# Kernel tuning notes

Hardware: AMD Instinct MI355X
Metric: run time of the kernel (lower is better)

The kernel has to match this reference:

```python
import jax, jax.numpy as jnp
import numpy as np

H = 4      # num_heads
C = 64     # attention_num_c
C_Z = 128  # num_in_c (pair rep channels)
C_T = 64   # num_in_c_kv (template pair channels)


def setup_inputs() -> dict:
    key = jax.random.key(0)
    ks = jax.random.split(key, 7)
    B, T, R = 1, 4, 384
    z2d = jax.random.normal(ks[0], (B, R, R, C_Z), dtype=jnp.float32)
    t2d = jax.random.normal(ks[1], (B, T, R, R, C_T), dtype=jnp.float32)
    s = 0.02
    Wq = jax.random.normal(ks[2], (C_Z, H * C), dtype=jnp.float32) * s
    Wk = jax.random.normal(ks[3], (C_T, H * C), dtype=jnp.float32) * s
    Wv = jax.random.normal(ks[4], (C_T, H * C), dtype=jnp.float32) * s
    Wo = jax.random.normal(ks[5], (H * C, C_Z), dtype=jnp.float32) * s
    bo = jax.random.normal(ks[6], (C_Z,), dtype=jnp.float32) * s
    return {"z2d": z2d, "t2d": t2d, "Wq": Wq, "Wk": Wk, "Wv": Wv, "Wo": Wo, "bo": bo}


def reference(z2d, t2d, Wq, Wk, Wv, Wo, bo):
    B, R = z2d.shape[0], z2d.shape[-2]
    T = t2d.shape[1]
    P = R * R  # residue-pair axis
    # query: one query per residue pair
    zq = z2d.reshape(B, P, 1, C_Z)
    # templates become the key/value axis per residue pair
    tkv = jnp.transpose(t2d, (0, 2, 3, 1, 4)).reshape(B, P, T, C_T)
    q = (zq @ Wq).reshape(B, P, 1, H, C) * (C ** -0.5)
    k = (tkv @ Wk).reshape(B, P, T, H, C)
    v = (tkv @ Wv).reshape(B, P, T, H, C)
    logits = jnp.einsum('bpqhc,bpkhc->bphqk', q, k)  # [B,P,H,1,T]
    weights = jax.nn.softmax(logits, axis=-1)
    weighted_avg = jnp.einsum('bphqk,bpkhc->bpqhc', weights, v)  # [B,P,1,H,C]
    out = weighted_avg.reshape(B, P, 1, H * C) @ Wo + bo
    return out.reshape(B, R, R, C_Z)
```

## Files before the change

kernel.cpp:

```cpp
#include <hip/hip_runtime.h>


#define R_    384
#define P_    (R_ * R_)
#define PB    32
#define NPB   256
#define NT_   18

typedef __attribute__((ext_vector_type(8))) short  short8;
typedef __attribute__((ext_vector_type(4))) float  f32x4;

union S8U { short8 s8; unsigned u[4]; };

__device__ __forceinline__ unsigned short f2bf(float f) {
  unsigned u = __float_as_uint(f);
  unsigned r = ((u >> 16) & 1u) + 0x7FFFu;
  return (unsigned short)((u + r) >> 16);
}
__device__ __forceinline__ float bf2f(unsigned short s) {
  return __uint_as_float(((unsigned)s) << 16);
}
__device__ __forceinline__ unsigned cvtpk(float lo, float hi) {
  unsigned d;
  asm("v_cvt_pk_bf16_f32 %0, %1, %2" : "=v"(d) : "v"(lo), "v"(hi));
  return d;
}
__device__ __forceinline__ int swz(int p, int c) {
  return p * 256 + ((((c >> 3) ^ (p & 31)) << 3) | (c & 7));
}
#define SB() __builtin_amdgcn_sched_barrier(0)
#define BAR() do { \
    asm volatile("s_waitcnt lgkmcnt(0)\ns_barrier" ::: "memory"); \
    SB(); \
  } while (0)

__device__ __forceinline__ void dma16(const float* g, void* lds) {
  __builtin_amdgcn_global_load_lds((const __attribute__((address_space(1))) unsigned*)g,
                                   (__attribute__((address_space(3))) unsigned*)lds,
                                   16, 0, 0);
}

__global__ void prep_kernel(const float* __restrict__ Wq, const float* __restrict__ Wk,
                            const float* __restrict__ Wv, const float* __restrict__ Wo,
                            unsigned short* __restrict__ AbarT,
                            unsigned short* __restrict__ MbarT) {
  int tid = blockIdx.x * blockDim.x + threadIdx.x;
  if (tid < 256 * 128) {
    int n = tid >> 7, i = tid & 127;
    int h = n >> 6, j = n & 63;
    const float* wq = Wq + i * 256 + h * 64;
    const float* wk = Wk + j * 256 + h * 64;
    float acc = 0.f;
#pragma unroll 8
    for (int c = 0; c < 64; ++c) acc += wq[c] * wk[c];
    AbarT[n * 128 + i] = f2bf(acc * 0.125f);
  } else {
    int t2 = tid - 256 * 128;
    int o = t2 >> 8, k = t2 & 255;
    int h = k >> 6, j = k & 63;
    const float* wv = Wv + j * 256 + h * 64;
    const float* wo = Wo + (h * 64) * 128 + o;
    float acc = 0.f;
#pragma unroll 8
    for (int c = 0; c < 64; ++c) acc += wv[c] * wo[c * 128];
    MbarT[o * 256 + k] = f2bf(acc);
  }
}

__global__ __launch_bounds__(512, 2) void attn_kernel(
    const float* __restrict__ z2d, const float* __restrict__ t2d,
    const unsigned short* __restrict__ AbarT, const unsigned short* __restrict__ MbarT,
    const float* __restrict__ bo, float* __restrict__ out) {
  extern __shared__ char smem[];
  unsigned short* sAbar = (unsigned short*)smem;
  float*          sTf   = (float*)(smem + 65536);
  unsigned short* sG    = (unsigned short*)(smem + 131072);

  const int tid  = threadIdx.x;
  const int wv_  = tid >> 6;
  const int lane = tid & 63;
  const int l = lane & 15;
  const int q = lane >> 4;
  const int mt = wv_ & 1;
  const int ng = wv_ >> 1;

  const int dp  = wv_ * 4 + (lane >> 4);
  const int dcf = (((lane & 15) ^ ((lane >> 4) & 3)) << 2);

  const int ap = tid >> 4, asub = tid & 15;
  const int ah = asub >> 2, au = asub & 3;
  const int aoG0 = swz(ap, ah * 64 + au * 16);
  const int aoG1 = swz(ap, ah * 64 + au * 16 + 8);
  int aoK[4];
#pragma unroll
  for (int j = 0; j < 4; ++j)
    aoK[j] = ap * 64 + ((((au * 4 + j) ^ (ap & 3))) << 2);

  const int p2g = mt * 16 + l;

#pragma unroll
  for (int k2 = 0; k2 < 8; ++k2) {
    int id = k2 * 512 + tid, n = id >> 4, blk = id & 15;
    short8 v = *(const short8*)(AbarT + n * 128 + blk * 8);
    *(short8*)(sAbar + n * 128 + ((blk ^ (n & 15)) << 3)) = v;
  }
  short8 mb0[8], mb1[8];
#pragma unroll
  for (int kk = 0; kk < 8; ++kk) {
    mb0[kk] = *(const short8*)(MbarT + (size_t)(ng * 32 + l) * 256 + kk * 32 + q * 8);
    mb1[kk] = *(const short8*)(MbarT + (size_t)(ng * 32 + 16 + l) * 256 + kk * 32 + q * 8);
  }
  const float bo0 = bo[ng * 32 + l];
  const float bo1 = bo[ng * 32 + 16 + l];
  SB();
  {
    const size_t P00 = (size_t)blockIdx.x * PB;
    char* dst = (char*)sTf + wv_ * 1024;
#pragma unroll
    for (int m = 0; m < 4; ++m)
      dma16(t2d + ((size_t)m * P_ + P00 + dp) * 64 + dcf, dst + m * 8192);
  }
  SB();
  float4 zb[8];
  {
    const float* zr = z2d + ((size_t)blockIdx.x * PB + mt * 16 + l) * 128;
#pragma unroll
    for (int kk = 0; kk < 4; ++kk) {
      zb[2 * kk]     = *(const float4*)(zr + kk * 32 + q * 8);
      zb[2 * kk + 1] = *(const float4*)(zr + kk * 32 + q * 8 + 4);
    }
  }
  BAR();

#pragma unroll 1
  for (int k = 0; k < NT_; ++k) {
    const int sl = k & 1;
    const size_t P0 = (size_t)(blockIdx.x + (size_t)k * NPB) * PB;
    const size_t P0n = P0 + (size_t)NPB * PB;

    if (k + 1 < NT_) {
      char* dst = (char*)sTf + (sl ^ 1) * 32768 + wv_ * 1024;
#pragma unroll
      for (int m = 0; m < 4; ++m)
        dma16(t2d + ((size_t)m * P_ + P0n + dp) * 64 + dcf, dst + m * 8192);
    }
    SB();
    if (k > 0) {
      const unsigned short* sGp = sG + (sl ^ 1) * 8192;
      f32x4 a20 = f32x4{0.f, 0.f, 0.f, 0.f};
      f32x4 a21 = f32x4{0.f, 0.f, 0.f, 0.f};
#pragma unroll
      for (int kk = 0; kk < 8; ++kk) {
        short8 af2 = *(const short8*)(sGp + p2g * 256 + (((kk * 4 + q) ^ p2g) << 3));
        a20 = __builtin_amdgcn_mfma_f32_16x16x32_bf16(af2, mb0[kk], a20, 0, 0, 0);
        a21 = __builtin_amdgcn_mfma_f32_16x16x32_bf16(af2, mb1[kk], a21, 0, 0, 0);
      }
      const size_t rb = (P0 - (size_t)NPB * PB + (size_t)(mt * 16 + q * 4)) * 128;
#pragma unroll
      for (int r = 0; r < 4; ++r) {
        out[rb + r * 128 + ng * 32 + l]      = a20[r] + bo0;
        out[rb + r * 128 + ng * 32 + 16 + l] = a21[r] + bo1;
      }
    }
    SB();
    {
      f32x4 a1[4];
#pragma unroll
      for (int i = 0; i < 4; ++i) a1[i] = f32x4{0.f, 0.f, 0.f, 0.f};
#pragma unroll
      for (int kk = 0; kk < 4; ++kk) {
        S8U af;
        af.u[0] = cvtpk(zb[2 * kk].x,     zb[2 * kk].y);
        af.u[1] = cvtpk(zb[2 * kk].z,     zb[2 * kk].w);
        af.u[2] = cvtpk(zb[2 * kk + 1].x, zb[2 * kk + 1].y);
        af.u[3] = cvtpk(zb[2 * kk + 1].z, zb[2 * kk + 1].w);
#pragma unroll
        for (int i = 0; i < 4; ++i) {
          const int n = (ng * 4 + i) * 16 + l;
          short8 bf = *(const short8*)(sAbar + n * 128 + (((kk * 4 + q) ^ l) << 3));
          a1[i] = __builtin_amdgcn_mfma_f32_16x16x32_bf16(af.s8, bf, a1[i], 0, 0, 0);
        }
      }
      unsigned short* sGc = sG + sl * 8192;
#pragma unroll
      for (int i = 0; i < 4; ++i) {
        const int c = (ng * 4 + i) * 16 + l;
#pragma unroll
        for (int r = 0; r < 4; ++r)
          sGc[swz(mt * 16 + q * 4 + r, c)] = f2bf(a1[i][r]);
      }
    }
    SB();
    if (k + 1 < NT_) {
      const float* zr = z2d + (P0n + (size_t)(mt * 16 + l)) * 128;
#pragma unroll
      for (int kk = 0; kk < 4; ++kk) {
        zb[2 * kk]     = *(const float4*)(zr + kk * 32 + q * 8);
        zb[2 * kk + 1] = *(const float4*)(zr + kk * 32 + q * 8 + 4);
      }
    }
    SB();
    BAR();

    {
      const float* Kt = sTf + sl * 8192;
      unsigned short* sGc = sG + sl * 8192;
      short8 g0 = *(const short8*)(sGc + aoG0);
      short8 g1 = *(const short8*)(sGc + aoG1);
      float lg0 = 0.f, lg1 = 0.f, lg2 = 0.f, lg3 = 0.f;
#pragma unroll
      for (int j = 0; j < 4; ++j) {
        const float ga = bf2f((unsigned short)((j < 2) ? g0[4 * j]     : g1[4 * (j - 2)]));
        const float gb = bf2f((unsigned short)((j < 2) ? g0[4 * j + 1] : g1[4 * (j - 2) + 1]));
        const float gc = bf2f((unsigned short)((j < 2) ? g0[4 * j + 2] : g1[4 * (j - 2) + 2]));
        const float gd = bf2f((unsigned short)((j < 2) ? g0[4 * j + 3] : g1[4 * (j - 2) + 3]));
        float4 k0 = *(const float4*)(Kt +        aoK[j]);
        float4 k1 = *(const float4*)(Kt + 2048 + aoK[j]);
        float4 k2 = *(const float4*)(Kt + 4096 + aoK[j]);
        float4 k3 = *(const float4*)(Kt + 6144 + aoK[j]);
        lg0 += ga * k0.x + gb * k0.y + gc * k0.z + gd * k0.w;
        lg1 += ga * k1.x + gb * k1.y + gc * k1.z + gd * k1.w;
        lg2 += ga * k2.x + gb * k2.y + gc * k2.z + gd * k2.w;
        lg3 += ga * k3.x + gb * k3.y + gc * k3.z + gd * k3.w;
      }
      lg0 += __shfl_xor(lg0, 1); lg0 += __shfl_xor(lg0, 2);
      lg1 += __shfl_xor(lg1, 1); lg1 += __shfl_xor(lg1, 2);
      lg2 += __shfl_xor(lg2, 1); lg2 += __shfl_xor(lg2, 2);
      lg3 += __shfl_xor(lg3, 1); lg3 += __shfl_xor(lg3, 2);
      const float mx = fmaxf(fmaxf(lg0, lg1), fmaxf(lg2, lg3));
      float e0 = __expf(lg0 - mx), e1 = __expf(lg1 - mx);
      float e2 = __expf(lg2 - mx), e3 = __expf(lg3 - mx);
      const float inv = 1.f / (e0 + e1 + e2 + e3);
      e0 *= inv; e1 *= inv; e2 *= inv; e3 *= inv;
#pragma unroll
      for (int j = 0; j < 4; ++j) {
        float4 k0 = *(const float4*)(Kt +        aoK[j]);
        float4 k1 = *(const float4*)(Kt + 2048 + aoK[j]);
        float4 k2 = *(const float4*)(Kt + 4096 + aoK[j]);
        float4 k3 = *(const float4*)(Kt + 6144 + aoK[j]);
        float s0 = e0 * k0.x + e1 * k1.x + e2 * k2.x + e3 * k3.x;
        float s1 = e0 * k0.y + e1 * k1.y + e2 * k2.y + e3 * k3.y;
        float s2 = e0 * k0.z + e1 * k1.z + e2 * k2.z + e3 * k3.z;
        float s3 = e0 * k0.w + e1 * k1.w + e2 * k2.w + e3 * k3.w;
        uint2 w2; w2.x = cvtpk(s0, s1); w2.y = cvtpk(s2, s3);
        *(uint2*)(sGc + swz(ap, ah * 64 + au * 16 + j * 4)) = w2;
      }
    }
    BAR();
  }

  {
    const unsigned short* sGp = sG + 8192;
    f32x4 a20 = f32x4{0.f, 0.f, 0.f, 0.f};
    f32x4 a21 = f32x4{0.f, 0.f, 0.f, 0.f};
#pragma unroll
    for (int kk = 0; kk < 8; ++kk) {
      short8 af2 = *(const short8*)(sGp + p2g * 256 + (((kk * 4 + q) ^ p2g) << 3));
      a20 = __builtin_amdgcn_mfma_f32_16x16x32_bf16(af2, mb0[kk], a20, 0, 0, 0);
      a21 = __builtin_amdgcn_mfma_f32_16x16x32_bf16(af2, mb1[kk], a21, 0, 0, 0);
    }
    const size_t rb = ((size_t)(blockIdx.x + (size_t)(NT_ - 1) * NPB) * PB
                       + (size_t)(mt * 16 + q * 4)) * 128;
#pragma unroll
    for (int r = 0; r < 4; ++r) {
      out[rb + r * 128 + ng * 32 + l]      = a20[r] + bo0;
      out[rb + r * 128 + ng * 32 + 16 + l] = a21[r] + bo1;
    }
  }
}

extern "C" void kernel_launch(void* const* d_in, const int* in_sizes, int n_in,
                              void* d_out, int out_size, void* d_ws, size_t ws_size,
                              hipStream_t stream) {
  const float* z2d = (const float*)d_in[0];
  const float* t2d = (const float*)d_in[1];
  const float* Wq  = (const float*)d_in[2];
  const float* Wk  = (const float*)d_in[3];
  const float* Wv  = (const float*)d_in[4];
  const float* Wo  = (const float*)d_in[5];
  const float* bo  = (const float*)d_in[6];

  unsigned short* AbarT = (unsigned short*)d_ws;
  unsigned short* MbarT = AbarT + 256 * 128;
  float* out = (float*)d_out;

  static bool attr_set = false;
  if (!attr_set) {
    (void)hipFuncSetAttribute((const void*)attn_kernel,
                              hipFuncAttributeMaxDynamicSharedMemorySize, 163840);
    attr_set = true;
  }

  hipLaunchKernelGGL(prep_kernel, dim3(256), dim3(256), 0, stream,
                     Wq, Wk, Wv, Wo, AbarT, MbarT);
  hipLaunchKernelGGL(attn_kernel, dim3(NPB), dim3(512), 163840, stream,
                     z2d, t2d, AbarT, MbarT, bo, out);
}
```

Baseline: 300.5 us.

## Keep Abar in registers and triple-buffer template tile DMA prefetch

The Abar projection matrix is now held in registers per wave instead of shared memory, which frees 64KB of LDS and removes per-iteration LDS reads for the first MFMA stage. The freed space goes to a third template-tile buffer, so the DMA prefetch runs two tiles ahead instead of one, hiding more global-load latency. The cost is higher register pressure (16 extra short8 per thread) at launch bounds of 512x2, which could cause spills.

```diff
diff --git a/kernel.cpp b/kernel.cpp
--- a/kernel.cpp
+++ b/kernel.cpp
@@ -72,9 +72,8 @@
     const unsigned short* __restrict__ AbarT, const unsigned short* __restrict__ MbarT,
     const float* __restrict__ bo, float* __restrict__ out) {
   extern __shared__ char smem[];
-  unsigned short* sAbar = (unsigned short*)smem;
-  float*          sTf   = (float*)(smem + 65536);
-  unsigned short* sG    = (unsigned short*)(smem + 131072);
+  float*          sTf = (float*)smem;
+  unsigned short* sG  = (unsigned short*)(smem + 98304);
 
   const int tid  = threadIdx.x;
   const int wv_  = tid >> 6;
@@ -98,12 +97,14 @@
 
   const int p2g = mt * 16 + l;
 
-#pragma unroll
-  for (int k2 = 0; k2 < 8; ++k2) {
-    int id = k2 * 512 + tid, n = id >> 4, blk = id & 15;
-    short8 v = *(const short8*)(AbarT + n * 128 + blk * 8);
-    *(short8*)(sAbar + n * 128 + ((blk ^ (n & 15)) << 3)) = v;
-  }
+  short8 ab[4][4];
+#pragma unroll
+  for (int kk = 0; kk < 4; ++kk)
+#pragma unroll
+    for (int i = 0; i < 4; ++i) {
+      const int n = (ng * 4 + i) * 16 + l;
+      ab[kk][i] = *(const short8*)(AbarT + n * 128 + kk * 32 + q * 8);
+    }
   short8 mb0[8], mb1[8];
 #pragma unroll
   for (int kk = 0; kk < 8; ++kk) {
@@ -115,10 +116,15 @@
   SB();
   {
     const size_t P00 = (size_t)blockIdx.x * PB;
-    char* dst = (char*)sTf + wv_ * 1024;
+    char* dst0 = (char*)sTf + wv_ * 1024;
 #pragma unroll
     for (int m = 0; m < 4; ++m)
-      dma16(t2d + ((size_t)m * P_ + P00 + dp) * 64 + dcf, dst + m * 8192);
+      dma16(t2d + ((size_t)m * P_ + P00 + dp) * 64 + dcf, dst0 + m * 8192);
+    const size_t P01 = P00 + (size_t)NPB * PB;
+    char* dst1 = (char*)sTf + 32768 + wv_ * 1024;
+#pragma unroll
+    for (int m = 0; m < 4; ++m)
+      dma16(t2d + ((size_t)m * P_ + P01 + dp) * 64 + dcf, dst1 + m * 8192);
   }
   SB();
   float4 zb[8];
@@ -134,19 +140,21 @@
 
 #pragma unroll 1
   for (int k = 0; k < NT_; ++k) {
-    const int sl = k & 1;
-    const size_t P0 = (size_t)(blockIdx.x + (size_t)k * NPB) * PB;
+    const int slT = (k % 3);
+    const int slG = k & 1;
+    const size_t P0  = (size_t)(blockIdx.x + (size_t)k * NPB) * PB;
     const size_t P0n = P0 + (size_t)NPB * PB;
 
-    if (k + 1 < NT_) {
-      char* dst = (char*)sTf + (sl ^ 1) * 32768 + wv_ * 1024;
+    if (k + 2 < NT_) {
+      char* dst = (char*)sTf + ((k + 2) % 3) * 32768 + wv_ * 1024;
+      const size_t P02 = P0 + 2 * (size_t)NPB * PB;
 #pragma unroll
       for (int m = 0; m < 4; ++m)
-        dma16(t2d + ((size_t)m * P_ + P0n + dp) * 64 + dcf, dst + m * 8192);
+        dma16(t2d + ((size_t)m * P_ + P02 + dp) * 64 + dcf, dst + m * 8192);
     }
     SB();
     if (k > 0) {
-      const unsigned short* sGp = sG + (sl ^ 1) * 8192;
+      const unsigned short* sGp = sG + (slG ^ 1) * 8192;
       f32x4 a20 = f32x4{0.f, 0.f, 0.f, 0.f};
       f32x4 a21 = f32x4{0.f, 0.f, 0.f, 0.f};
 #pragma unroll
@@ -175,13 +183,10 @@
         af.u[2] = cvtpk(zb[2 * kk + 1].x, zb[2 * kk + 1].y);
         af.u[3] = cvtpk(zb[2 * kk + 1].z, zb[2 * kk + 1].w);
 #pragma unroll
-        for (int i = 0; i < 4; ++i) {
-          const int n = (ng * 4 + i) * 16 + l;
-          short8 bf = *(const short8*)(sAbar + n * 128 + (((kk * 4 + q) ^ l) << 3));
-          a1[i] = __builtin_amdgcn_mfma_f32_16x16x32_bf16(af.s8, bf, a1[i], 0, 0, 0);
-        }
-      }
-      unsigned short* sGc = sG + sl * 8192;
+        for (int i = 0; i < 4; ++i)
+          a1[i] = __builtin_amdgcn_mfma_f32_16x16x32_bf16(af.s8, ab[kk][i], a1[i], 0, 0, 0);
+      }
+      unsigned short* sGc = sG + slG * 8192;
 #pragma unroll
       for (int i = 0; i < 4; ++i) {
         const int c = (ng * 4 + i) * 16 + l;
@@ -203,8 +208,8 @@
     BAR();
 
     {
-      const float* Kt = sTf + sl * 8192;
-      unsigned short* sGc = sG + sl * 8192;
+      const float* Kt = sTf + slT * 8192;
+      unsigned short* sGc = sG + slG * 8192;
       short8 g0 = *(const short8*)(sGc + aoG0);
       short8 g1 = *(const short8*)(sGc + aoG1);
       float lg0 = 0.f, lg1 = 0.f, lg2 = 0.f, lg3 = 0.f;
@@ -287,12 +292,12 @@
   static bool attr_set = false;
   if (!attr_set) {
     (void)hipFuncSetAttribute((const void*)attn_kernel,
-                              hipFuncAttributeMaxDynamicSharedMemorySize, 163840);
+                              hipFuncAttributeMaxDynamicSharedMemorySize, 131072);
     attr_set = true;
   }
 
   hipLaunchKernelGGL(prep_kernel, dim3(256), dim3(256), 0, stream,
                      Wq, Wk, Wv, Wo, AbarT, MbarT);
-  hipLaunchKernelGGL(attn_kernel, dim3(NPB), dim3(512), 163840, stream,
+  hipLaunchKernelGGL(attn_kernel, dim3(NPB), dim3(512), 131072, stream,
                      z2d, t2d, AbarT, MbarT, bo, out);
 }
```

After: 308.1 us. +2.5%, slower.

## Load template K/V tiles directly into registers instead of LDS DMA

Applied to the files above, without the earlier changes.

Replaces the global_load_lds double-buffered staging of template features in LDS with direct per-thread float4 global loads into a 64-register array, prefetched one tile ahead at the end of each iteration. This removes the LDS traffic and footprint for the template tile, cutting shared memory from 160KB to 96KB. The cost is much higher register pressure (64 extra VGPRs for the prefetch) under launch bounds of 512 threads with 2 blocks, which risks spills. Prefetch latency is now hidden only by the barrier and the next iteration's MFMA work.

```diff
diff --git a/kernel.cpp b/kernel.cpp
--- a/kernel.cpp
+++ b/kernel.cpp
@@ -33,12 +33,6 @@
     asm volatile("s_waitcnt lgkmcnt(0)\ns_barrier" ::: "memory"); \
     SB(); \
   } while (0)
-
-__device__ __forceinline__ void dma16(const float* g, void* lds) {
-  __builtin_amdgcn_global_load_lds((const __attribute__((address_space(1))) unsigned*)g,
-                                   (__attribute__((address_space(3))) unsigned*)lds,
-                                   16, 0, 0);
-}
 
 __global__ void prep_kernel(const float* __restrict__ Wq, const float* __restrict__ Wk,
                             const float* __restrict__ Wv, const float* __restrict__ Wo,
@@ -73,8 +67,7 @@
     const float* __restrict__ bo, float* __restrict__ out) {
   extern __shared__ char smem[];
   unsigned short* sAbar = (unsigned short*)smem;
-  float*          sTf   = (float*)(smem + 65536);
-  unsigned short* sG    = (unsigned short*)(smem + 131072);
+  unsigned short* sG    = (unsigned short*)(smem + 65536);
 
   const int tid  = threadIdx.x;
   const int wv_  = tid >> 6;
@@ -84,17 +77,10 @@
   const int mt = wv_ & 1;
   const int ng = wv_ >> 1;
 
-  const int dp  = wv_ * 4 + (lane >> 4);
-  const int dcf = (((lane & 15) ^ ((lane >> 4) & 3)) << 2);
-
   const int ap = tid >> 4, asub = tid & 15;
   const int ah = asub >> 2, au = asub & 3;
   const int aoG0 = swz(ap, ah * 64 + au * 16);
   const int aoG1 = swz(ap, ah * 64 + au * 16 + 8);
-  int aoK[4];
-#pragma unroll
-  for (int j = 0; j < 4; ++j)
-    aoK[j] = ap * 64 + ((((au * 4 + j) ^ (ap & 3))) << 2);
 
   const int p2g = mt * 16 + l;
 
@@ -113,12 +99,14 @@
   const float bo0 = bo[ng * 32 + l];
   const float bo1 = bo[ng * 32 + 16 + l];
   SB();
+  float4 kt[4][4];
   {
-    const size_t P00 = (size_t)blockIdx.x * PB;
-    char* dst = (char*)sTf + wv_ * 1024;
-#pragma unroll
-    for (int m = 0; m < 4; ++m)
-      dma16(t2d + ((size_t)m * P_ + P00 + dp) * 64 + dcf, dst + m * 8192);
+    const float* kb = t2d + ((size_t)blockIdx.x * PB + ap) * 64 + au * 16;
+#pragma unroll
+    for (int t = 0; t < 4; ++t)
+#pragma unroll
+      for (int j = 0; j < 4; ++j)
+        kt[t][j] = *(const float4*)(kb + (size_t)t * (P_ * 64) + 4 * j);
   }
   SB();
   float4 zb[8];
@@ -135,16 +123,9 @@
 #pragma unroll 1
   for (int k = 0; k < NT_; ++k) {
     const int sl = k & 1;
-    const size_t P0 = (size_t)(blockIdx.x + (size_t)k * NPB) * PB;
+    const size_t P0  = (size_t)(blockIdx.x + (size_t)k * NPB) * PB;
     const size_t P0n = P0 + (size_t)NPB * PB;
 
-    if (k + 1 < NT_) {
-      char* dst = (char*)sTf + (sl ^ 1) * 32768 + wv_ * 1024;
-#pragma unroll
-      for (int m = 0; m < 4; ++m)
-        dma16(t2d + ((size_t)m * P_ + P0n + dp) * 64 + dcf, dst + m * 8192);
-    }
-    SB();
     if (k > 0) {
       const unsigned short* sGp = sG + (sl ^ 1) * 8192;
       f32x4 a20 = f32x4{0.f, 0.f, 0.f, 0.f};
@@ -203,7 +184,6 @@
     BAR();
 
     {
-      const float* Kt = sTf + sl * 8192;
       unsigned short* sGc = sG + sl * 8192;
       short8 g0 = *(const short8*)(sGc + aoG0);
       short8 g1 = *(const short8*)(sGc + aoG1);
@@ -214,14 +194,10 @@
         const float gb = bf2f((unsigned short)((j < 2) ? g0[4 * j + 1] : g1[4 * (j - 2) + 1]));
         const float gc = bf2f((unsigned short)((j < 2) ? g0[4 * j + 2] : g1[4 * (j - 2) + 2]));
         const float gd = bf2f((unsigned short)((j < 2) ? g0[4 * j + 3] : g1[4 * (j - 2) + 3]));
-        float4 k0 = *(const float4*)(Kt +        aoK[j]);
-        float4 k1 = *(const float4*)(Kt + 2048 + aoK[j]);
-        float4 k2 = *(const float4*)(Kt + 4096 + aoK[j]);
-        float4 k3 = *(const float4*)(Kt + 6144 + aoK[j]);
-        lg0 += ga * k0.x + gb * k0.y + gc * k0.z + gd * k0.w;
-        lg1 += ga * k1.x + gb * k1.y + gc * k1.z + gd * k1.w;
-        lg2 += ga * k2.x + gb * k2.y + gc * k2.z + gd * k2.w;
-        lg3 += ga * k3.x + gb * k3.y + gc * k3.z + gd * k3.w;
+        lg0 += ga * kt[0][j].x + gb * kt[0][j].y + gc * kt[0][j].z + gd * kt[0][j].w;
+        lg1 += ga * kt[1][j].x + gb * kt[1][j].y + gc * kt[1][j].z + gd * kt[1][j].w;
+        lg2 += ga * kt[2][j].x + gb * kt[2][j].y + gc * kt[2][j].z + gd * kt[2][j].w;
+        lg3 += ga * kt[3][j].x + gb * kt[3][j].y + gc * kt[3][j].z + gd * kt[3][j].w;
       }
       lg0 += __shfl_xor(lg0, 1); lg0 += __shfl_xor(lg0, 2);
       lg1 += __shfl_xor(lg1, 1); lg1 += __shfl_xor(lg1, 2);
@@ -234,18 +210,24 @@
       e0 *= inv; e1 *= inv; e2 *= inv; e3 *= inv;
 #pragma unroll
       for (int j = 0; j < 4; ++j) {
-        float4 k0 = *(const float4*)(Kt +        aoK[j]);
-        float4 k1 = *(const float4*)(Kt + 2048 + aoK[j]);
-        float4 k2 = *(const float4*)(Kt + 4096 + aoK[j]);
-        float4 k3 = *(const float4*)(Kt + 6144 + aoK[j]);
-        float s0 = e0 * k0.x + e1 * k1.x + e2 * k2.x + e3 * k3.x;
-        float s1 = e0 * k0.y + e1 * k1.y + e2 * k2.y + e3 * k3.y;
-        float s2 = e0 * k0.z + e1 * k1.z + e2 * k2.z + e3 * k3.z;
-        float s3 = e0 * k0.w + e1 * k1.w + e2 * k2.w + e3 * k3.w;
+        float s0 = e0 * kt[0][j].x + e1 * kt[1][j].x + e2 * kt[2][j].x + e3 * kt[3][j].x;
+        float s1 = e0 * kt[0][j].y + e1 * kt[1][j].y + e2 * kt[2][j].y + e3 * kt[3][j].y;
+        float s2 = e0 * kt[0][j].z + e1 * kt[1][j].z + e2 * kt[2][j].z + e3 * kt[3][j].z;
+        float s3 = e0 * kt[0][j].w + e1 * kt[1][j].w + e2 * kt[2][j].w + e3 * kt[3][j].w;
         uint2 w2; w2.x = cvtpk(s0, s1); w2.y = cvtpk(s2, s3);
-        *(uint2*)(sGc + swz(ap, ah * 64 + au * 16 + j * 4)) = w2;
-      }
-    }
+        *(uint2*)(sGc + swz(ap, ah * 64 + au * 16 + 4 * j)) = w2;
+      }
+    }
+    SB();
+    if (k + 1 < NT_) {
+      const float* kb = t2d + (P0n + ap) * 64 + au * 16;
+#pragma unroll
+      for (int t = 0; t < 4; ++t)
+#pragma unroll
+        for (int j = 0; j < 4; ++j)
+          kt[t][j] = *(const float4*)(kb + (size_t)t * (P_ * 64) + 4 * j);
+    }
+    SB();
     BAR();
   }
 
@@ -287,12 +269,12 @@
   static bool attr_set = false;
   if (!attr_set) {
     (void)hipFuncSetAttribute((const void*)attn_kernel,
-                              hipFuncAttributeMaxDynamicSharedMemorySize, 163840);
+                              hipFuncAttributeMaxDynamicSharedMemorySize, 98304);
     attr_set = true;
   }
 
   hipLaunchKernelGGL(prep_kernel, dim3(256), dim3(256), 0, stream,
                      Wq, Wk, Wv, Wo, AbarT, MbarT);
-  hipLaunchKernelGGL(attn_kernel, dim3(NPB), dim3(512), 163840, stream,
+  hipLaunchKernelGGL(attn_kernel, dim3(NPB), dim3(512), 98304, stream,
                      z2d, t2d, AbarT, MbarT, bo, out);
 }
```

Measured after the change: 310.7 us. +3.4%, slower.
